# Performance work log

Hardware: AMD Instinct MI355X
Metric: run time of the kernel (lower is better)

Reference implementation:

```python
import jax, jax.numpy as jnp
import numpy as np

B, N, C, H = 8, 2048, 256, 4
RES = 2048
OUT_C = 1


def _split_heads(t, h):
    b, n, hd = t.shape
    return t.reshape(b, n, h, hd // h).transpose(0, 2, 1, 3)


def _merge_heads(t):
    b, h, n, d = t.shape
    return t.transpose(0, 2, 1, 3).reshape(b, n, h * d)


def _inst_norm(x, eps=1e-5):
    # torch InstanceNorm1d applied per-token over head dim, no affine, biased var
    mu = jnp.mean(x, -1, keepdims=True)
    var = jnp.mean((x - mu) ** 2, -1, keepdims=True)
    return (x - mu) / jnp.sqrt(var + eps)


def _layer_norm(x, g, b, eps=1e-5):
    mu = jnp.mean(x, -1, keepdims=True)
    var = jnp.mean((x - mu) ** 2, -1, keepdims=True)
    return (x - mu) / jnp.sqrt(var + eps) * g + b


def _rot_half(x):
    d = x.shape[-1] // 2
    return jnp.concatenate([-x[..., d:], x[..., :d]], axis=-1)


def _rotary_freqs(coords, dim, mult):
    # RotaryEmbedding: t * (scale/min_freq), outer with inv_freq, cat(f, f)
    inv = 1.0 / (10000.0 ** (jnp.arange(0, dim, 2, dtype=jnp.float32) / dim))
    f = (coords * mult)[..., None] * inv  # [..., dim//2]
    return jnp.concatenate([f, f], axis=-1)


def _apply_rot(t, f):
    return t * jnp.cos(f) + _rot_half(t) * jnp.sin(f)


def _gelu(x):
    return jax.nn.gelu(x, approximate=False)


def setup_inputs():
    key = jax.random.key(0)
    ks = jax.random.split(key, 20)
    def rn(k, shp, s=0.02):
        return jax.random.normal(k, shp, dtype=jnp.float32) * s
    return {
        "z": jax.random.normal(ks[0], (B, N, C), jnp.float32),
        "propagate_pos": jax.random.uniform(ks[1], (B, N, 1), jnp.float32),
        # Gaussian Fourier feature matrix (fixed, scale=8)
        "B_fourier": jax.random.normal(ks[2], (1, C), jnp.float32) * 8.0,
        "W_coord": rn(ks[3], (2 * C, C)),
        # CrossLinearAttention (heads=4, dim_head=C, project_query=False)
        "W_kv": rn(ks[4], (C, 2 * H * C)),
        "Wo_ca": rn(ks[5], (H * C, C)),
        "bo_ca": jnp.zeros((C,), jnp.float32),
        # CrossFormer FFN (mlp_dim=C)
        "Wf1": rn(ks[6], (C, C)), "bf1": jnp.zeros((C,), jnp.float32),
        "Wf2": rn(ks[7], (C, C)), "bf2": jnp.zeros((C,), jnp.float32),
        # propagator: LayerNorm + 3-layer GELU MLP (no biases)
        "ln_g": jnp.ones((C,), jnp.float32), "ln_b": jnp.zeros((C,), jnp.float32),
        "P1": rn(ks[8], (C + 1, C)), "P2": rn(ks[9], (C, C)), "P3": rn(ks[10], (C, C)),
        # decode LinearAttention (heads=1, dim_head=C)
        "W_qkv": rn(ks[11], (C, 3 * C)),
        "Wo_da": rn(ks[12], (C, C)), "bo_da": jnp.zeros((C,), jnp.float32),
        # decode FFN
        "ln2_g": jnp.ones((C,), jnp.float32), "ln2_b": jnp.zeros((C,), jnp.float32),
        "D1": rn(ks[13], (C, C)), "D2": rn(ks[14], (C, C // 2)),
        "D3": rn(ks[15], (C // 2, OUT_C)), "b3": jnp.zeros((OUT_C,), jnp.float32),
    }


def reference(z, propagate_pos, B_fourier, W_coord, W_kv, Wo_ca, bo_ca,
              Wf1, bf1, Wf2, bf2, ln_g, ln_b, P1, P2, P3,
              W_qkv, Wo_da, bo_da, ln2_g, ln2_b, D1, D2, D3, b3):
    pos = propagate_pos  # [B, N, 1]
    n = z.shape[1]
    # --- coordinate projection: Gaussian Fourier features -> GELU -> Linear ---
    xp = 2.0 * np.pi * ((pos / 16.0) @ B_fourier)            # [B, N, C]
    feat = jnp.concatenate([jnp.sin(xp), jnp.cos(xp)], -1)   # [B, N, 2C]
    x = _gelu(feat) @ W_coord                                # [B, N, C]
    # --- cross linear attention ('fourier', heads=4, dim_head=C, q unprojected) ---
    k, v = jnp.split(z @ W_kv, 2, axis=-1)
    k = _split_heads(k, H)
    v = _split_heads(v, H)                                   # [B, H, N, C]
    q = jnp.broadcast_to(x[:, None], (x.shape[0], H, n, C))  # repeat query over heads
    q = _inst_norm(q)
    k = _inst_norm(k)
    f = _rotary_freqs(pos[..., 0], C, float(RES))[:, None]   # scale/min_freq = res
    q = _apply_rot(q, f)
    k = _apply_rot(k, f)                                     # z_pos=None -> same freqs
    dots = jnp.einsum('bhnd,bhne->bhde', k, v)               # [B, H, C, C]
    out = jnp.einsum('bhnd,bhde->bhne', q, dots) / n
    x = _merge_heads(out) @ Wo_ca + bo_ca + x
    # --- CrossFormer FFN + residual ---
    x = _gelu(x @ Wf1 + bf1) @ Wf2 + bf2 + x
    # --- propagator: LN, concat(pos/16), 3-layer GELU MLP, residual ---
    h = jnp.concatenate([_layer_norm(x, ln_g, ln_b), pos / 16.0], -1)
    zp = _gelu(_gelu(h @ P1) @ P2) @ P3 + x
    # --- decode: linear self-attention (heads=1, fourier) + FFN ---
    q2, k2, v2 = jnp.split(zp @ W_qkv, 3, axis=-1)           # each [B, N, C]
    q2 = _inst_norm(q2)
    k2 = _inst_norm(k2)
    f2 = _rotary_freqs(pos[..., 0], C, float(RES))
    q2 = _apply_rot(q2, f2)
    k2 = _apply_rot(k2, f2)
    dots2 = jnp.einsum('bnd,bne->bde', k2, v2)               # [B, C, C]
    att = jnp.einsum('bnd,bde->bne', q2, dots2) / n
    zd = att @ Wo_da + bo_da + zp
    h2 = _layer_norm(zd, ln2_g, ln2_b)
    u = _gelu(_gelu(h2 @ D1) @ D2) @ D3 + b3                 # [B, N, OUT_C]
    u = jnp.transpose(u, (0, 2, 1))                          # 'b n (t c) -> b (t c) n', t=1
    return (u, zp)
```

## Files before the change

### kernel.cpp

```cpp
#include <hip/hip_runtime.h>
#include <hip/hip_bf16.h>

using bf16 = __hip_bfloat16;
typedef __attribute__((ext_vector_type(8))) short short8;
typedef __attribute__((ext_vector_type(4))) short short4v;
typedef __attribute__((ext_vector_type(4))) float f32x4;

constexpr int BB = 8;
constexpr int NN = 2048;
constexpr int CC = 256;
constexpr int NTOK = BB * NN;
constexpr float TWO_PI = 6.283185307179586f;
constexpr float LOG2_1E4 = 13.287712379549449f;

__device__ __forceinline__ float gelu_f(float x) {
  return 0.5f * x * (1.0f + erff(x * 0.7071067811865475f));
}

template <int T>
__device__ __forceinline__ void stats_rows(const float (*buf)[CC], float* mu, float* rs, float eps) {
  __syncthreads();
  int w = threadIdx.x >> 6, l = threadIdx.x & 63;
  if (w < T) {
    float s = 0.f, s2 = 0.f;
#pragma unroll
    for (int j = 0; j < 4; ++j) { float v = buf[w][l + 64 * j]; s += v; s2 += v * v; }
#pragma unroll
    for (int o = 32; o; o >>= 1) { s += __shfl_down(s, o); s2 += __shfl_down(s2, o); }
    if (l == 0) {
      float m = s * (1.f / 256.f);
      float var = fmaxf(s2 * (1.f / 256.f) - m * m, 0.f);
      mu[w] = m; rs[w] = rsqrtf(var + eps);
    }
  }
  __syncthreads();
}

#define GLD16(src, dst)                                                       \
  __builtin_amdgcn_global_load_lds(                                           \
      (const __attribute__((address_space(1))) void*)(src),                   \
      (__attribute__((address_space(3))) void*)(dst), 16, 0, 0)

template <int K, int MI>
__device__ __forceinline__ void gemm_core(
    const bf16* __restrict__ Ap, int lda, const bf16* __restrict__ Bp,
    bf16 (&As)[MI * 32 * 64], bf16 (&Bs)[64 * 64], f32x4 (&acc)[MI][2]) {
  const int tid = threadIdx.x;
  const int w = tid >> 6, l = tid & 63;
  const int srow = l >> 3;
  const int scol = ((l & 7) ^ srow) * 8;
  const int rsw = (l & 7) * 8;
  const int wm = w >> 1, wn = w & 1;
  for (int kt = 0; kt < K; kt += 64) {
#pragma unroll
    for (int i = 0; i < MI; ++i) {
      int r = (w * MI + i) * 8 + srow;
      GLD16(Ap + (long)r * lda + kt + scol, &As[(w * MI + i) * 512 + l * 8]);
    }
#pragma unroll
    for (int i = 0; i < 2; ++i) {
      int r = (w * 2 + i) * 8 + srow;
      GLD16(Bp + (long)r * K + kt + scol, &Bs[(w * 2 + i) * 512 + l * 8]);
    }
    __syncthreads();
    short8 bfr[2][2];
#pragma unroll
    for (int ni = 0; ni < 2; ++ni)
#pragma unroll
      for (int ks = 0; ks < 2; ++ks)
        bfr[ni][ks] = *(const short8*)&Bs[(wn * 32 + ni * 16 + (l & 15)) * 64 +
                                          ((ks * 32 + (l >> 4) * 8) ^ rsw)];
#pragma unroll
    for (int mi = 0; mi < MI; ++mi) {
#pragma unroll
      for (int ks = 0; ks < 2; ++ks) {
        short8 afr = *(const short8*)&As[(wm * (MI * 16) + mi * 16 + (l & 15)) * 64 +
                                         ((ks * 32 + (l >> 4) * 8) ^ rsw)];
#pragma unroll
        for (int ni = 0; ni < 2; ++ni)
          acc[mi][ni] = __builtin_amdgcn_mfma_f32_16x16x32_bf16(afr, bfr[ni][ks], acc[mi][ni], 0, 0, 0);
      }
    }
    __syncthreads();
  }
}

enum { E_BF16 = 0, E_BIAS_RESB_BOTH, E_BIAS_GELU, E_BIAS_RES_F32,
       E_RANK1_GELU, E_GELU, E_RES_BOTH };

template <int K, int EPI>
__global__ void __launch_bounds__(256) k_gemm(
    const bf16* __restrict__ A, int lda, const bf16* __restrict__ Bt,
    long bstride, long zstride, int nOffZ,
    const float* __restrict__ bias, const float* __restrict__ res,
    const bf16* __restrict__ resB, const float* __restrict__ rank1,
    const float* __restrict__ pvec,
    float* __restrict__ outF, bf16* __restrict__ outB, int ldo) {
  __shared__ bf16 As[128 * 64];
  __shared__ bf16 Bs[64 * 64];
  const int tid = threadIdx.x;
  const int w = tid >> 6, l = tid & 63;
  const int m0 = blockIdx.y * 128, n0 = blockIdx.x * 64;
  const int bidx = m0 >> 11;
  const bf16* Bp = Bt + (long)bidx * bstride + (long)blockIdx.z * zstride + (long)n0 * K;
  f32x4 acc[4][2] = {};
  gemm_core<K, 4>(A + (long)m0 * lda, lda, Bp, As, Bs, acc);
  const int wm = w >> 1, wn = w & 1;
  const int zoff = blockIdx.z * nOffZ;
#pragma unroll
  for (int mi = 0; mi < 4; ++mi) {
#pragma unroll
    for (int ni = 0; ni < 2; ++ni) {
      const int bcol = n0 + wn * 32 + ni * 16 + (l & 15);
      const int ocol = bcol + zoff;
#pragma unroll
      for (int r = 0; r < 4; ++r) {
        const int row = m0 + wm * 64 + mi * 16 + (l >> 4) * 4 + r;
        float v = acc[mi][ni][r];
        const long oidx = (long)row * ldo + ocol;
        if constexpr (EPI == E_BF16) { outB[oidx] = __float2bfloat16(v); }
        else if constexpr (EPI == E_BIAS_RESB_BOTH) {
          v += bias[bcol] + __bfloat162float(resB[oidx]);
          outF[oidx] = v; outB[oidx] = __float2bfloat16(v);
        } else if constexpr (EPI == E_BIAS_GELU) {
          v = gelu_f(v + bias[bcol]); outB[oidx] = __float2bfloat16(v);
        } else if constexpr (EPI == E_BIAS_RES_F32) {
          v += bias[bcol] + res[oidx]; outF[oidx] = v;
        } else if constexpr (EPI == E_RANK1_GELU) {
          v = gelu_f(v + pvec[row] * rank1[bcol]); outB[oidx] = __float2bfloat16(v);
        } else if constexpr (EPI == E_GELU) {
          v = gelu_f(v); outB[oidx] = __float2bfloat16(v);
        } else {
          v += res[oidx]; outF[oidx] = v; outB[oidx] = __float2bfloat16(v);
        }
      }
    }
  }
}

template <int K>
__global__ void __launch_bounds__(256) k_gemmT(
    const bf16* __restrict__ A, int lda, const bf16* __restrict__ Bt,
    bf16* __restrict__ T0, bf16* __restrict__ T1, int thresh, int matsPerB) {
  __shared__ union {
    struct { bf16 A[128 * 64]; bf16 B[64 * 64]; } ab;
    bf16 stage[64 * 132];
  } sm;
  const int tid = threadIdx.x;
  const int w = tid >> 6, l = tid & 63;
  const int m0 = blockIdx.y * 128, n0 = blockIdx.x * 64;
  f32x4 acc[4][2] = {};
  gemm_core<K, 4>(A + (long)m0 * lda, lda, Bt + (long)n0 * K, sm.ab.A, sm.ab.B, acc);
  const int wm = w >> 1, wn = w & 1;
#pragma unroll
  for (int mi = 0; mi < 4; ++mi)
#pragma unroll
    for (int ni = 0; ni < 2; ++ni) {
      int c = wn * 32 + ni * 16 + (l & 15);
      int row0 = wm * 64 + mi * 16 + (l >> 4) * 4;
#pragma unroll
      for (int q = 0; q < 2; ++q) {
        bf16 b0 = __float2bfloat16(acc[mi][ni][2 * q]);
        bf16 b1 = __float2bfloat16(acc[mi][ni][2 * q + 1]);
        unsigned u = (unsigned)*(unsigned short*)&b0 |
                     ((unsigned)*(unsigned short*)&b1 << 16);
        *(unsigned*)&sm.stage[c * 132 + row0 + 2 * q] = u;
      }
    }
  __syncthreads();
  const int b = m0 >> 11, nbase = m0 & 2047;
  const int part = (n0 >= thresh) ? 1 : 0;
  const int cT0 = n0 - (part ? thresh : 0);
  bf16* dst = (part ? T1 : T0) + ((long)(b * matsPerB + (cT0 >> 8))) * 524288
            + (long)(cT0 & 255) * 2048;
  const int c = tid >> 2, ns = tid & 3;
  bf16* rowp = dst + (long)c * 2048 + nbase + ns * 32;
#pragma unroll
  for (int j = 0; j < 4; ++j) {
    short4v lo = *(const short4v*)&sm.stage[c * 132 + ns * 32 + j * 8];
    short4v hi = *(const short4v*)&sm.stage[c * 132 + ns * 32 + j * 8 + 4];
    short8 v;
    v[0] = lo[0]; v[1] = lo[1]; v[2] = lo[2]; v[3] = lo[3];
    v[4] = hi[0]; v[5] = hi[1]; v[6] = hi[2]; v[7] = hi[3];
    *(short8*)&rowp[j * 8] = v;
  }
}

template <int MI>
__global__ void __launch_bounds__(256) k_atb2(
    const bf16* __restrict__ A0, const bf16* __restrict__ B0,
    bf16* __restrict__ D0, float scale) {
  __shared__ bf16 As[MI * 32 * 64];
  __shared__ bf16 Bs[64 * 64];
  const int tid = threadIdx.x;
  const int w = tid >> 6, l = tid & 63;
  const int mat = blockIdx.z;
  const int m0 = blockIdx.y * (MI * 32), n0 = blockIdx.x * 64;
  const bf16* Ap = A0 + (long)mat * 524288 + (long)m0 * 2048;
  const bf16* Bp = B0 + (long)mat * 524288 + (long)n0 * 2048;
  f32x4 acc[MI][2] = {};
  gemm_core<2048, MI>(Ap, 2048, Bp, As, Bs, acc);
  bf16* D = D0 + (long)mat * 65536;
  const int wm = w >> 1, wn = w & 1;
#pragma unroll
  for (int mi = 0; mi < MI; ++mi)
#pragma unroll
    for (int ni = 0; ni < 2; ++ni) {
      int col = n0 + wn * 32 + ni * 16 + (l & 15);
#pragma unroll
      for (int r = 0; r < 4; ++r) {
        int row = m0 + wm * (MI * 16) + mi * 16 + (l >> 4) * 4 + r;
        D[(long)row * 256 + col] = __float2bfloat16(acc[mi][ni][r] * scale);
      }
    }
}

__global__ void __launch_bounds__(256) k_stats(
    const bf16* __restrict__ Kt, float* __restrict__ mu, float* __restrict__ rs) {
  const int mat = blockIdx.y;
  const int n = blockIdx.x * 256 + threadIdx.x;
  const bf16* base = Kt + (long)mat * 524288 + n;
  float s = 0.f, s2 = 0.f;
#pragma unroll 4
  for (int c = 0; c < 256; ++c) {
    float v = __bfloat162float(base[(long)c * 2048]);
    s += v; s2 += v * v;
  }
  float m = s * (1.f / 256.f);
  mu[(long)mat * 2048 + n] = m;
  rs[(long)mat * 2048 + n] = rsqrtf(fmaxf(s2 * (1.f / 256.f) - m * m, 0.f) + 1e-5f);
}

__global__ void __launch_bounds__(256) k_rotnorm(
    bf16* __restrict__ Kt, const float* __restrict__ mu, const float* __restrict__ rs,
    const bf16* __restrict__ csT, int hshift) {
  const int mat = blockIdx.y, c = blockIdx.x;
  const int n = threadIdx.x * 8;
  const int b = mat >> hshift;
  bf16* r0 = Kt + (long)mat * 524288 + (long)c * 2048 + n;
  bf16* r1 = r0 + 128 * 2048;
  const long tok = (long)b * 2048 + n;
  const bf16* cop = csT + ((long)c * 2) * 16384 + tok;
  const bf16* sip = cop + 16384;
  const float* mup = mu + (long)mat * 2048 + n;
  const float* rsp = rs + (long)mat * 2048 + n;
  short8 v0 = *(const short8*)r0, v1 = *(const short8*)r1;
  short8 co8 = *(const short8*)cop, si8 = *(const short8*)sip;
  short8 o0, o1;
#pragma unroll
  for (int e = 0; e < 8; ++e) {
    float m = mup[e], r = rsp[e];
    float a = (__uint_as_float(((unsigned)(unsigned short)v0[e]) << 16) - m) * r;
    float bb = (__uint_as_float(((unsigned)(unsigned short)v1[e]) << 16) - m) * r;
    float co = __uint_as_float(((unsigned)(unsigned short)co8[e]) << 16);
    float si = __uint_as_float(((unsigned)(unsigned short)si8[e]) << 16);
    bf16 t0 = __float2bfloat16(a * co - bb * si);
    bf16 t1 = __float2bfloat16(bb * co + a * si);
    o0[e] = *(short*)&t0; o1[e] = *(short*)&t1;
  }
  *(short8*)r0 = o0;
  *(short8*)r1 = o1;
}

__global__ void __launch_bounds__(256) k_rotq(
    const bf16* __restrict__ in, bf16* __restrict__ out, const bf16* __restrict__ cs) {
  __shared__ float xr[4][CC];
  __shared__ float mu[4], rs[4];
  int tid = threadIdx.x;
  long tok0 = (long)blockIdx.x * 4;
#pragma unroll
  for (int t = 0; t < 4; ++t) xr[t][tid] = __bfloat162float(in[(tok0 + t) * 256 + tid]);
  stats_rows<4>(xr, mu, rs, 1e-5f);
  int i = tid & 127;
#pragma unroll
  for (int t = 0; t < 4; ++t) {
    float co = __bfloat162float(cs[(tok0 + t) * 256 + i]);
    float si = __bfloat162float(cs[(tok0 + t) * 256 + 128 + i]);
    float n0 = (xr[t][tid] - mu[t]) * rs[t];
    float n1 = (xr[t][tid ^ 128] - mu[t]) * rs[t];
    float o = (tid < 128) ? (n0 * co - n1 * si) : (n0 * co + n1 * si);
    out[(tok0 + t) * 256 + tid] = __float2bfloat16(o);
  }
}

struct WEnt { const float* s; bf16* d; int K; int N; int blk0; };
struct WTab { WEnt e[12]; };

__global__ void __launch_bounds__(256) k_wprep(WTab t) {
  int bid = blockIdx.x;
  int ei = 0;
#pragma unroll
  for (int i = 1; i < 12; ++i)
    if (bid >= t.e[i].blk0) ei = i;
  WEnt e = t.e[ei];
  int local = (bid - e.blk0) * 256 + threadIdx.x;
  if (local < e.K * e.N) {
    int n = local / e.K, k = local - n * e.K;
    e.d[local] = __float2bfloat16(e.s[(long)k * e.N + n]);
  }
}

__global__ void __launch_bounds__(256) k_pre(
    const float* __restrict__ pos, const float* __restrict__ Bf,
    const float* __restrict__ z, const float* __restrict__ P1,
    bf16* __restrict__ gf, bf16* __restrict__ cs, bf16* __restrict__ csT,
    float* __restrict__ pvec, bf16* __restrict__ zb, float* __restrict__ P1L) {
  int tid = threadIdx.x;
  long tok0 = (long)blockIdx.x * 4;
  if (blockIdx.x == 0) P1L[tid] = P1[65536 + tid];
  float p[4];
#pragma unroll
  for (int t = 0; t < 4; ++t) p[t] = pos[tok0 + t];
  if (tid < 4) pvec[tok0 + tid] = p[tid] * 0.0625f;
  float bfc = Bf[tid];
#pragma unroll
  for (int t = 0; t < 4; ++t) {
    float xp = TWO_PI * (p[t] * 0.0625f) * bfc;
    float s, c; sincosf(xp, &s, &c);
    gf[(tok0 + t) * 512 + tid] = __float2bfloat16(gelu_f(s));
    gf[(tok0 + t) * 512 + 256 + tid] = __float2bfloat16(gelu_f(c));
    zb[(tok0 + t) * 256 + tid] = __float2bfloat16(z[(tok0 + t) * 256 + tid]);
  }
  if (tid < 128) {
    float inv = exp2f(-((float)tid * (1.f / 128.f)) * LOG2_1E4);
#pragma unroll
    for (int t = 0; t < 4; ++t) {
      float fh = p[t] * 2048.f * inv;
      float s, c; sincosf(fh, &s, &c);
      bf16 cb = __float2bfloat16(c), sb = __float2bfloat16(s);
      cs[(tok0 + t) * 256 + tid] = cb;
      cs[(tok0 + t) * 256 + 128 + tid] = sb;
      csT[(long)(tid * 2) * 16384 + tok0 + t] = cb;
      csT[(long)(tid * 2 + 1) * 16384 + tok0 + t] = sb;
    }
  }
}

__global__ void __launch_bounds__(256) k_ln(
    const float* __restrict__ xin, const float* __restrict__ g,
    const float* __restrict__ b, bf16* __restrict__ hout) {
  __shared__ float xr[4][CC];
  __shared__ float mu[4], rs[4];
  int tid = threadIdx.x;
  long tok0 = (long)blockIdx.x * 4;
#pragma unroll
  for (int t = 0; t < 4; ++t) xr[t][tid] = xin[(tok0 + t) * 256 + tid];
  stats_rows<4>(xr, mu, rs, 1e-5f);
  float gv = g[tid], bv = b[tid];
#pragma unroll
  for (int t = 0; t < 4; ++t)
    hout[(tok0 + t) * 256 + tid] = __float2bfloat16((xr[t][tid] - mu[t]) * rs[t] * gv + bv);
}

__global__ void __launch_bounds__(256) k_final(
    const bf16* __restrict__ g2, const float* __restrict__ D3,
    const float* __restrict__ b3, float* __restrict__ u) {
  int w = threadIdx.x >> 6, l = threadIdx.x & 63;
  long tok = (long)blockIdx.x * 4 + w;
  float s = __bfloat162float(g2[tok * 128 + l]) * D3[l]
          + __bfloat162float(g2[tok * 128 + 64 + l]) * D3[64 + l];
#pragma unroll
  for (int o = 32; o; o >>= 1) s += __shfl_down(s, o);
  if (l == 0) u[tok] = s + b3[0];
}

extern "C" void kernel_launch(void* const* d_in, const int* in_sizes, int n_in,
                              void* d_out, int out_size, void* d_ws, size_t ws_size,
                              hipStream_t stream) {
  const float* z    = (const float*)d_in[0];
  const float* pos  = (const float*)d_in[1];
  const float* Bf   = (const float*)d_in[2];
  const float* Wc   = (const float*)d_in[3];
  const float* Wkv  = (const float*)d_in[4];
  const float* Woca = (const float*)d_in[5];
  const float* boca = (const float*)d_in[6];
  const float* Wf1  = (const float*)d_in[7];
  const float* bf1  = (const float*)d_in[8];
  const float* Wf2  = (const float*)d_in[9];
  const float* bf2  = (const float*)d_in[10];
  const float* lng  = (const float*)d_in[11];
  const float* lnb  = (const float*)d_in[12];
  const float* P1   = (const float*)d_in[13];
  const float* P2   = (const float*)d_in[14];
  const float* P3   = (const float*)d_in[15];
  const float* Wqkv = (const float*)d_in[16];
  const float* Woda = (const float*)d_in[17];
  const float* boda = (const float*)d_in[18];
  const float* ln2g = (const float*)d_in[19];
  const float* ln2b = (const float*)d_in[20];
  const float* D1   = (const float*)d_in[21];
  const float* D2   = (const float*)d_in[22];
  const float* D3   = (const float*)d_in[23];
  const float* b3   = (const float*)d_in[24];

  float* u  = (float*)d_out;
  float* zp = (float*)d_out + NTOK;

  const long MB = 1048576L;
  char* ws = (char*)d_ws;
  bf16*  cs   = (bf16*)(ws);
  bf16*  csT  = (bf16*)(ws + 8 * MB);
  float* pvec = (float*)(ws + 16 * MB);
  long wo = 16 * MB + 65536;
  bf16* WcT   = (bf16*)(ws + wo);               wo += 262144;
  bf16* WkvT  = (bf16*)(ws + wo);               wo += 1048576;
  bf16* WocaT = (bf16*)(ws + wo);               wo += 524288;
  bf16* Wf1T  = (bf16*)(ws + wo);               wo += 131072;
  bf16* Wf2T  = (bf16*)(ws + wo);               wo += 131072;
  bf16* P1T   = (bf16*)(ws + wo);               wo += 131072;
  bf16* P2T   = (bf16*)(ws + wo);               wo += 131072;
  bf16* P3T   = (bf16*)(ws + wo);               wo += 131072;
  bf16* WqkvT = (bf16*)(ws + wo);               wo += 393216;
  bf16* WodaT = (bf16*)(ws + wo);               wo += 131072;
  bf16* D1T   = (bf16*)(ws + wo);               wo += 131072;
  bf16* D2T   = (bf16*)(ws + wo);               wo += 65536;
  float* P1L  = (float*)(ws + wo);              wo += 1024;
  float* muB  = (float*)(ws + wo);              wo += 32 * 2048 * 4;
  float* rsB  = (float*)(ws + wo);              wo += 32 * 2048 * 4;
  char* AR = ws + 24 * MB;
  bf16*  xb     = (bf16*)(AR);
  bf16*  zb     = (bf16*)(AR + 8 * MB);
  bf16*  gf     = (bf16*)(AR + 48 * MB);
  bf16*  Kt     = (bf16*)(AR + 16 * MB);
  bf16*  Vt     = (bf16*)(AR + 48 * MB);
  bf16*  dotsT  = (bf16*)(AR + 8 * MB);
  bf16*  qrot   = (bf16*)(AR + 16 * MB);
  bf16*  merged = (bf16*)(AR + 24 * MB);
  float* x2     = (float*)(AR + 56 * MB);
  bf16*  x2b    = (bf16*)(AR + 72 * MB);
  bf16*  t1     = (bf16*)(AR + 8 * MB);
  float* x3     = (float*)(AR + 16 * MB);
  bf16*  h      = (bf16*)(AR + 32 * MB);
  bf16*  p1o    = (bf16*)(AR + 40 * MB);
  bf16*  p2o    = (bf16*)(AR + 48 * MB);
  bf16*  zpb    = (bf16*)(AR + 56 * MB);
  bf16*  q2b    = (bf16*)(AR + 64 * MB);
  bf16*  k2t    = (bf16*)(AR + 72 * MB);
  bf16*  v2t    = (bf16*)(AR + 8 * MB);
  bf16*  dots2T = (bf16*)(AR + 16 * MB);
  bf16*  att    = (bf16*)(AR + 24 * MB);
  float* zd     = (float*)(AR + 32 * MB);
  bf16*  h2     = (bf16*)(AR + 8 * MB);
  bf16*  g1     = (bf16*)(AR + 16 * MB);
  bf16*  g2     = (bf16*)(AR + 24 * MB);

  WTab tab;
  int nb = 0;
  auto add = [&](int i, const float* s, bf16* d, int K_, int N_) {
    tab.e[i].s = s; tab.e[i].d = d; tab.e[i].K = K_; tab.e[i].N = N_;
    tab.e[i].blk0 = nb; nb += (K_ * N_) / 256;
  };
  add(0, Wc, WcT, 512, 256);
  add(1, Wkv, WkvT, 256, 2048);
  add(2, Woca, WocaT, 1024, 256);
  add(3, Wf1, Wf1T, 256, 256);
  add(4, Wf2, Wf2T, 256, 256);
  add(5, P1, P1T, 256, 256);
  add(6, P2, P2T, 256, 256);
  add(7, P3, P3T, 256, 256);
  add(8, Wqkv, WqkvT, 256, 768);
  add(9, Woda, WodaT, 256, 256);
  add(10, D1, D1T, 256, 256);
  add(11, D2, D2T, 256, 128);
  k_wprep<<<nb, 256, 0, stream>>>(tab);

  k_pre<<<NTOK / 4, 256, 0, stream>>>(pos, Bf, z, P1, gf, cs, csT, pvec, zb, P1L);
  k_gemm<512, E_BF16><<<dim3(4, 128, 1), 256, 0, stream>>>(
      gf, 512, WcT, 0, 0, 0, nullptr, nullptr, nullptr, nullptr, nullptr, nullptr, xb, 256);
  k_gemmT<256><<<dim3(32, 128), 256, 0, stream>>>(zb, 256, WkvT, Kt, Vt, 1024, 4);
  k_stats<<<dim3(8, 32), 256, 0, stream>>>(Kt, muB, rsB);
  k_rotnorm<<<dim3(128, 32), 256, 0, stream>>>(Kt, muB, rsB, csT, 2);
  k_atb2<4><<<dim3(4, 2, 32), 256, 0, stream>>>(Vt, Kt, dotsT, 1.f / 2048.f);
  k_rotq<<<NTOK / 4, 256, 0, stream>>>(xb, qrot, cs);
  k_gemm<256, E_BF16><<<dim3(4, 128, 4), 256, 0, stream>>>(
      qrot, 256, dotsT, 262144L, 65536L, 256, nullptr, nullptr, nullptr, nullptr, nullptr,
      nullptr, merged, 1024);
  k_gemm<1024, E_BIAS_RESB_BOTH><<<dim3(4, 128, 1), 256, 0, stream>>>(
      merged, 1024, WocaT, 0, 0, 0, boca, nullptr, xb, nullptr, nullptr, x2, x2b, 256);
  k_gemm<256, E_BIAS_GELU><<<dim3(4, 128, 1), 256, 0, stream>>>(
      x2b, 256, Wf1T, 0, 0, 0, bf1, nullptr, nullptr, nullptr, nullptr, nullptr, t1, 256);
  k_gemm<256, E_BIAS_RES_F32><<<dim3(4, 128, 1), 256, 0, stream>>>(
      t1, 256, Wf2T, 0, 0, 0, bf2, x2, nullptr, nullptr, nullptr, x3, nullptr, 256);
  k_ln<<<NTOK / 4, 256, 0, stream>>>(x3, lng, lnb, h);
  k_gemm<256, E_RANK1_GELU><<<dim3(4, 128, 1), 256, 0, stream>>>(
      h, 256, P1T, 0, 0, 0, nullptr, nullptr, nullptr, P1L, pvec, nullptr, p1o, 256);
  k_gemm<256, E_GELU><<<dim3(4, 128, 1), 256, 0, stream>>>(
      p1o, 256, P2T, 0, 0, 0, nullptr, nullptr, nullptr, nullptr, nullptr, nullptr, p2o, 256);
  k_gemm<256, E_RES_BOTH><<<dim3(4, 128, 1), 256, 0, stream>>>(
      p2o, 256, P3T, 0, 0, 0, nullptr, x3, nullptr, nullptr, nullptr, zp, zpb, 256);
  k_gemm<256, E_BF16><<<dim3(4, 128, 1), 256, 0, stream>>>(
      zpb, 256, WqkvT, 0, 0, 0, nullptr, nullptr, nullptr, nullptr, nullptr, nullptr, q2b, 256);
  k_gemmT<256><<<dim3(8, 128), 256, 0, stream>>>(zpb, 256, WqkvT + 65536, k2t, v2t, 256, 1);
  k_rotq<<<NTOK / 4, 256, 0, stream>>>(q2b, q2b, cs);
  k_stats<<<dim3(8, 8), 256, 0, stream>>>(k2t, muB, rsB);
  k_rotnorm<<<dim3(128, 8), 256, 0, stream>>>(k2t, muB, rsB, csT, 0);
  k_atb2<2><<<dim3(4, 4, 8), 256, 0, stream>>>(v2t, k2t, dots2T, 1.f / 2048.f);
  k_gemm<256, E_BF16><<<dim3(4, 128, 1), 256, 0, stream>>>(
      q2b, 256, dots2T, 65536L, 0, 0, nullptr, nullptr, nullptr, nullptr, nullptr,
      nullptr, att, 256);
  k_gemm<256, E_BIAS_RES_F32><<<dim3(4, 128, 1), 256, 0, stream>>>(
      att, 256, WodaT, 0, 0, 0, boda, zp, nullptr, nullptr, nullptr, zd, nullptr, 256);
  k_ln<<<NTOK / 4, 256, 0, stream>>>(zd, ln2g, ln2b, h2);
  k_gemm<256, E_GELU><<<dim3(4, 128, 1), 256, 0, stream>>>(
      h2, 256, D1T, 0, 0, 0, nullptr, nullptr, nullptr, nullptr, nullptr, nullptr, g1, 256);
  k_gemm<256, E_GELU><<<dim3(2, 128, 1), 256, 0, stream>>>(
      g1, 256, D2T, 0, 0, 0, nullptr, nullptr, nullptr, nullptr, nullptr, nullptr, g2, 128);
  k_final<<<NTOK / 4, 256, 0, stream>>>(g2, D3, b3, u);
}
```

Measured before the change: 476.6 us.

## Double-buffer GEMM LDS tiles and move transposed rotary table to coalesced kernel

The shared GEMM core now uses two LDS buffers per operand, issuing the next K-tile's global-to-LDS loads before computing on the current tile so memory latency overlaps with MFMA work. This doubles LDS usage per block, which may lower occupancy. Separately, the transposed cos/sin table, previously written with strided 2-byte stores from the preprocessing kernel, is now produced by a dedicated kernel whose threads map to consecutive tokens, giving coalesced writes at the cost of one extra launch and recomputing the sincos.

```diff
diff --git a/kernel.cpp b/kernel.cpp
--- a/kernel.cpp
+++ b/kernel.cpp
@@ -44,44 +44,56 @@
 template <int K, int MI>
 __device__ __forceinline__ void gemm_core(
     const bf16* __restrict__ Ap, int lda, const bf16* __restrict__ Bp,
-    bf16 (&As)[MI * 32 * 64], bf16 (&Bs)[64 * 64], f32x4 (&acc)[MI][2]) {
+    bf16 (&As)[2][MI * 32 * 64], bf16 (&Bs)[2][64 * 64], f32x4 (&acc)[MI][2]) {
   const int tid = threadIdx.x;
   const int w = tid >> 6, l = tid & 63;
   const int srow = l >> 3;
   const int scol = ((l & 7) ^ srow) * 8;
   const int rsw = (l & 7) * 8;
   const int wm = w >> 1, wn = w & 1;
-  for (int kt = 0; kt < K; kt += 64) {
+
+  auto stage_tile = [&](int buf, int kt) {
 #pragma unroll
     for (int i = 0; i < MI; ++i) {
       int r = (w * MI + i) * 8 + srow;
-      GLD16(Ap + (long)r * lda + kt + scol, &As[(w * MI + i) * 512 + l * 8]);
+      GLD16(Ap + (long)r * lda + kt + scol, &As[buf][(w * MI + i) * 512 + l * 8]);
     }
 #pragma unroll
     for (int i = 0; i < 2; ++i) {
       int r = (w * 2 + i) * 8 + srow;
-      GLD16(Bp + (long)r * K + kt + scol, &Bs[(w * 2 + i) * 512 + l * 8]);
-    }
-    __syncthreads();
+      GLD16(Bp + (long)r * K + kt + scol, &Bs[buf][(w * 2 + i) * 512 + l * 8]);
+    }
+  };
+
+  stage_tile(0, 0);
+  asm volatile("s_waitcnt vmcnt(0)" ::: "memory");
+  __builtin_amdgcn_s_barrier();
+
+  int cur = 0;
+  for (int kt = 0; kt < K; kt += 64) {
+    const bool more = (kt + 64 < K);
+    if (more) stage_tile(cur ^ 1, kt + 64);
     short8 bfr[2][2];
 #pragma unroll
     for (int ni = 0; ni < 2; ++ni)
 #pragma unroll
       for (int ks = 0; ks < 2; ++ks)
-        bfr[ni][ks] = *(const short8*)&Bs[(wn * 32 + ni * 16 + (l & 15)) * 64 +
-                                          ((ks * 32 + (l >> 4) * 8) ^ rsw)];
+        bfr[ni][ks] = *(const short8*)&Bs[cur][(wn * 32 + ni * 16 + (l & 15)) * 64 +
+                                               ((ks * 32 + (l >> 4) * 8) ^ rsw)];
 #pragma unroll
     for (int mi = 0; mi < MI; ++mi) {
 #pragma unroll
       for (int ks = 0; ks < 2; ++ks) {
-        short8 afr = *(const short8*)&As[(wm * (MI * 16) + mi * 16 + (l & 15)) * 64 +
-                                         ((ks * 32 + (l >> 4) * 8) ^ rsw)];
+        short8 afr = *(const short8*)&As[cur][(wm * (MI * 16) + mi * 16 + (l & 15)) * 64 +
+                                              ((ks * 32 + (l >> 4) * 8) ^ rsw)];
 #pragma unroll
         for (int ni = 0; ni < 2; ++ni)
           acc[mi][ni] = __builtin_amdgcn_mfma_f32_16x16x32_bf16(afr, bfr[ni][ks], acc[mi][ni], 0, 0, 0);
       }
     }
-    __syncthreads();
+    if (more) asm volatile("s_waitcnt vmcnt(0)" ::: "memory");
+    __builtin_amdgcn_s_barrier();
+    cur ^= 1;
   }
 }
 
@@ -96,8 +108,8 @@
     const bf16* __restrict__ resB, const float* __restrict__ rank1,
     const float* __restrict__ pvec,
     float* __restrict__ outF, bf16* __restrict__ outB, int ldo) {
-  __shared__ bf16 As[128 * 64];
-  __shared__ bf16 Bs[64 * 64];
+  __shared__ bf16 As[2][128 * 64];
+  __shared__ bf16 Bs[2][64 * 64];
   const int tid = threadIdx.x;
   const int w = tid >> 6, l = tid & 63;
   const int m0 = blockIdx.y * 128, n0 = blockIdx.x * 64;
@@ -143,7 +155,7 @@
     const bf16* __restrict__ A, int lda, const bf16* __restrict__ Bt,
     bf16* __restrict__ T0, bf16* __restrict__ T1, int thresh, int matsPerB) {
   __shared__ union {
-    struct { bf16 A[128 * 64]; bf16 B[64 * 64]; } ab;
+    struct { bf16 A[2][128 * 64]; bf16 B[2][64 * 64]; } ab;
     bf16 stage[64 * 132];
   } sm;
   const int tid = threadIdx.x;
@@ -190,8 +202,8 @@
 __global__ void __launch_bounds__(256) k_atb2(
     const bf16* __restrict__ A0, const bf16* __restrict__ B0,
     bf16* __restrict__ D0, float scale) {
-  __shared__ bf16 As[MI * 32 * 64];
-  __shared__ bf16 Bs[64 * 64];
+  __shared__ bf16 As[2][MI * 32 * 64];
+  __shared__ bf16 Bs[2][64 * 64];
   const int tid = threadIdx.x;
   const int w = tid >> 6, l = tid & 63;
   const int mat = blockIdx.z;
@@ -300,10 +312,21 @@
   }
 }
 
+__global__ void __launch_bounds__(256) k_csT(
+    const float* __restrict__ pos, bf16* __restrict__ csT) {
+  const int c = blockIdx.y;
+  const int n = blockIdx.x * 256 + threadIdx.x;
+  float inv = exp2f(-((float)c * (1.f / 128.f)) * LOG2_1E4);
+  float fh = pos[n] * 2048.f * inv;
+  float s, co; sincosf(fh, &s, &co);
+  csT[(long)(c * 2) * 16384 + n] = __float2bfloat16(co);
+  csT[(long)(c * 2 + 1) * 16384 + n] = __float2bfloat16(s);
+}
+
 __global__ void __launch_bounds__(256) k_pre(
     const float* __restrict__ pos, const float* __restrict__ Bf,
     const float* __restrict__ z, const float* __restrict__ P1,
-    bf16* __restrict__ gf, bf16* __restrict__ cs, bf16* __restrict__ csT,
+    bf16* __restrict__ gf, bf16* __restrict__ cs,
     float* __restrict__ pvec, bf16* __restrict__ zb, float* __restrict__ P1L) {
   int tid = threadIdx.x;
   long tok0 = (long)blockIdx.x * 4;
@@ -327,11 +350,8 @@
     for (int t = 0; t < 4; ++t) {
       float fh = p[t] * 2048.f * inv;
       float s, c; sincosf(fh, &s, &c);
-      bf16 cb = __float2bfloat16(c), sb = __float2bfloat16(s);
-      cs[(tok0 + t) * 256 + tid] = cb;
-      cs[(tok0 + t) * 256 + 128 + tid] = sb;
-      csT[(long)(tid * 2) * 16384 + tok0 + t] = cb;
-      csT[(long)(tid * 2 + 1) * 16384 + tok0 + t] = sb;
+      cs[(tok0 + t) * 256 + tid] = __float2bfloat16(c);
+      cs[(tok0 + t) * 256 + 128 + tid] = __float2bfloat16(s);
     }
   }
 }
@@ -464,7 +484,8 @@
   add(11, D2, D2T, 256, 128);
   k_wprep<<<nb, 256, 0, stream>>>(tab);
 
-  k_pre<<<NTOK / 4, 256, 0, stream>>>(pos, Bf, z, P1, gf, cs, csT, pvec, zb, P1L);
+  k_pre<<<NTOK / 4, 256, 0, stream>>>(pos, Bf, z, P1, gf, cs, pvec, zb, P1L);
+  k_csT<<<dim3(NTOK / 256, 128), 256, 0, stream>>>(pos, csT);
   k_gemm<512, E_BF16><<<dim3(4, 128, 1), 256, 0, stream>>>(
       gf, 512, WcT, 0, 0, 0, nullptr, nullptr, nullptr, nullptr, nullptr, nullptr, xb, 256);
   k_gemmT<256><<<dim3(32, 128), 256, 0, stream>>>(zb, 256, WkvT, Kt, Vt, 1024, 4);
```

Result: faster. 464.9 us (-2.5%).
